# Kernel tuning notes

Hardware: AMD Instinct MI355X
Metric: run time of the kernel (lower is better)

## Reference

```python
import jax, jax.numpy as jnp
import numpy as np

L = 3          # layers
D = 256        # hidden_dim
H = 4          # heads
F = 1024       # ffn_size
IMG = (64, 32) # img_dim
S = IMG[0] * IMG[1]
DK = D // H    # key/query head dim
V = 2 * D      # double_v_dim value dim
DV = V // H    # value head dim
B = 2


def _rel_pos():
    # rotary angles, repeated pairwise as in get_rel_pos
    angle = 1.0 / (10000.0 ** jnp.linspace(0.0, 1.0, DK // 2))
    angle = jnp.repeat(angle, 2)                                  # [DK]
    idx = jnp.arange(S, dtype=jnp.float32)
    sin = jnp.sin(idx[:, None] * angle[None, :])                  # [S, DK]
    cos = jnp.cos(idx[:, None] * angle[None, :])
    # per-head causal decay mask, row-normalized by sqrt(rowsum)
    decay = jnp.log(1.0 - 2.0 ** (-5.0 - jnp.arange(H, dtype=jnp.float32)))  # [H]
    diff = idx[:, None] - idx[None, :]                            # [S, S]
    mask = jnp.where(diff >= 0, jnp.exp(diff[None, :, :] * decay[:, None, None]), 0.0)
    mask = mask / jnp.sqrt(mask.sum(-1, keepdims=True))           # [H, S, S]
    return sin, cos, mask


def _theta_shift(x, sin, cos):
    # x: [B, H, S, DK]; rotate-every-two rotary embedding
    x1, x2 = x[..., ::2], x[..., 1::2]
    rot = jnp.stack([-x2, x1], axis=-1).reshape(x.shape)
    return x * cos + rot * sin


def _ln(x, w, b, eps=1e-5):
    mu = x.mean(-1, keepdims=True)
    var = ((x - mu) ** 2).mean(-1, keepdims=True)
    return (x - mu) / jnp.sqrt(var + eps) * w + b


def _retention(x, sin, cos, mask, Wq, Wk, Wv, Wg, Wo):
    b, s, _ = x.shape
    q = (x @ Wq).reshape(b, s, H, DK).transpose(0, 2, 1, 3)
    k = (x @ Wk).reshape(b, s, H, DK).transpose(0, 2, 1, 3) * (DK ** -0.5)
    v = (x @ Wv).reshape(b, s, H, DV).transpose(0, 2, 1, 3)
    g = x @ Wg                                                    # [b, s, V]
    qr = _theta_shift(q, sin, cos)
    kr = _theta_shift(k, sin, cos)
    qk = jnp.einsum('bhsd,bhtd->bhst', qr, kr) * mask[None]
    denom = jnp.clip(jnp.abs(qk).sum(-1, keepdims=True), 1.0, None)
    qk = qk / jax.lax.stop_gradient(denom)
    o = jnp.einsum('bhst,bhtv->bhsv', qk, v)                      # [b, H, s, DV]
    o = o * jax.lax.rsqrt((o ** 2).mean(-1, keepdims=True) + 1e-6)  # per-head RMSNorm
    o = o.transpose(0, 2, 1, 3).reshape(b, s, V)
    o = (g * jax.nn.sigmoid(g)) * o                               # swish gate
    return o @ Wo


def setup_inputs():
    key = jax.random.key(0)
    ks = jax.random.split(key, 16)
    sc = 0.02
    return {
        'x': jax.random.normal(ks[0], (B, S, D), jnp.float32),
        'Wq': jax.random.normal(ks[1], (L, D, D), jnp.float32) * sc,
        'Wk': jax.random.normal(ks[2], (L, D, D), jnp.float32) * sc,
        'Wv': jax.random.normal(ks[3], (L, D, V), jnp.float32) * sc,
        'Wg': jax.random.normal(ks[4], (L, D, V), jnp.float32) * sc,
        'Wo': jax.random.normal(ks[5], (L, V, D), jnp.float32) * sc,
        'ln1_w': jnp.ones((L, D), jnp.float32),
        'ln1_b': jnp.zeros((L, D), jnp.float32),
        'ln2_w': jnp.ones((L, D), jnp.float32),
        'ln2_b': jnp.zeros((L, D), jnp.float32),
        'W1': jax.random.normal(ks[6], (L, D, F), jnp.float32) * sc,
        'b1': jnp.zeros((L, F), jnp.float32),
        'W2': jax.random.normal(ks[7], (L, F, D), jnp.float32) * sc,
        'b2': jnp.zeros((L, D), jnp.float32),
    }


def reference(x, Wq, Wk, Wv, Wg, Wo, ln1_w, ln1_b, ln2_w, ln2_b, W1, b1, W2, b2):
    sin, cos, mask = _rel_pos()
    for i in range(L):
        y = _retention(_ln(x, ln1_w[i], ln1_b[i]), sin, cos, mask,
                       Wq[i], Wk[i], Wv[i], Wg[i], Wo[i]) + x
        h = _ln(y, ln2_w[i], ln2_b[i])
        x = (jax.nn.gelu(h @ W1[i] + b1[i], approximate=False) @ W2[i] + b2[i]) + y
    return x.reshape(x.shape[0], IMG[0], IMG[1], D)
```

## Files before the change

### kernel.cpp

```cpp
#include <hip/hip_runtime.h>
#include <hip/hip_bf16.h>
#include <cstddef>
#include <cmath>
#include <algorithm>

#define SEQ 2048
#define DMODEL 256
#define NHEAD 4
#define DK 64
#define VDIM 512
#define DV 128
#define NB 2
#define FDIM 1024
#define NROWS (NB*SEQ)
#define QKVGN 1536
#define NSLOT 144

typedef unsigned short u16;
typedef __attribute__((ext_vector_type(8))) short short8;
typedef __attribute__((ext_vector_type(4))) short short4v;
typedef __attribute__((ext_vector_type(4))) float f32x4;

static __device__ __forceinline__ u16 f2b(float f) {
    union { float f; unsigned u; } c; c.f = f;
    unsigned r = c.u + 0x7fffu + ((c.u >> 16) & 1u);
    return (u16)(r >> 16);
}
static __device__ __forceinline__ float b2f(u16 u) {
    union { unsigned u; float f; } c; c.u = ((unsigned)u) << 16; return c.f;
}

static __device__ __forceinline__ f32x4 mfma16_bf16(short4v a, short4v b, f32x4 c) {
    return __builtin_amdgcn_mfma_f32_16x16x16bf16_1k(a, b, c, 0, 0, 0);
}

static __device__ __forceinline__ short4v pack_bf16x4(float a0, float a1, float a2, float a3) {
    union { short4v v; unsigned u[2]; } z;
    union { __hip_bfloat162 h; unsigned u; } p0, p1;
    p0.h = __float22bfloat162_rn(make_float2(a0, a1));
    p1.h = __float22bfloat162_rn(make_float2(a2, a3));
    z.u[0] = p0.u; z.u[1] = p1.u;
    return z.v;
}

#define GLOAD_LDS16(GP, LP) \
    __builtin_amdgcn_global_load_lds((const __attribute__((address_space(1))) void*)(GP), \
                                     (__attribute__((address_space(3))) void*)(LP), 16, 0, 0)

__global__ void tables_kernel(float* __restrict__ sint, float* __restrict__ cost)
{
    int idx = blockIdx.x * 256 + threadIdx.x;
    if (idx >= SEQ * DK) return;
    int s = idx >> 6, d = idx & 63;
    int j = d >> 1;
    float a = powf(10000.f, -(float)j / 31.f);
    float arg = (float)s * a;
    sint[idx] = sinf(arg);
    cost[idx] = cosf(arg);
}

__global__ __launch_bounds__(256) void wconv_kernel(const float* __restrict__ in,
                                                    u16* __restrict__ out, int K, int N,
                                                    size_t in_lstride, size_t out_lstride)
{
    __shared__ float tile[32][33];
    int n0 = blockIdx.x * 32, k0 = blockIdx.y * 32;
    const float* inz = in + (size_t)blockIdx.z * in_lstride;
    u16* outz = out + (size_t)blockIdx.z * out_lstride;
    int tx = threadIdx.x, ty = threadIdx.y;
    #pragma unroll
    for (int r = 0; r < 4; ++r) {
        int kr = ty + r * 8;
        tile[kr][tx] = inz[(size_t)(k0 + kr) * N + n0 + tx];
    }
    __syncthreads();
    #pragma unroll
    for (int r = 0; r < 4; ++r) {
        int nr = ty + r * 8;
        outz[(size_t)(n0 + nr) * K + k0 + tx] = f2b(tile[tx][nr]);
    }
}

__global__ __launch_bounds__(256) void ln_kernel(const float* __restrict__ x,
                                                 const float* __restrict__ w,
                                                 const float* __restrict__ b,
                                                 u16* __restrict__ o)
{
    int row = blockIdx.x * 4 + (threadIdx.x >> 6);
    int lane = threadIdx.x & 63;
    size_t base = (size_t)row * DMODEL + lane * 4;
    f32x4 v = *(const f32x4*)(x + base);
    float s  = v[0] + v[1] + v[2] + v[3];
    float s2 = v[0]*v[0] + v[1]*v[1] + v[2]*v[2] + v[3]*v[3];
    #pragma unroll
    for (int st = 1; st < 64; st <<= 1) { s += __shfl_xor(s, st); s2 += __shfl_xor(s2, st); }
    float mu = s * (1.f / 256.f);
    float var = s2 * (1.f / 256.f) - mu * mu;
    float rstd = rsqrtf(var + 1e-5f);
    f32x4 wv = *(const f32x4*)(w + lane * 4);
    f32x4 bv = *(const f32x4*)(b + lane * 4);
    f32x4 r = (v - mu) * rstd * wv + bv;
    *(short4v*)(o + base) = pack_bf16x4(r[0], r[1], r[2], r[3]);
}

template<int NPART, int HASBIAS>
__global__ __launch_bounds__(256) void lncomb_kernel(const u16* __restrict__ pW,
                                                     const float* __restrict__ bias,
                                                     const float* __restrict__ res,
                                                     const float* __restrict__ w,
                                                     const float* __restrict__ b,
                                                     float* __restrict__ yout,
                                                     u16* __restrict__ o)
{
    int row = blockIdx.x * 4 + (threadIdx.x >> 6);
    int lane = threadIdx.x & 63;
    size_t base = (size_t)row * DMODEL + lane * 4;
    const size_t PS = (size_t)NROWS * DMODEL;
    f32x4 v = *(const f32x4*)(res + base);
    #pragma unroll
    for (int k = 0; k < NPART; ++k) {
        short4v sv = *(const short4v*)(pW + base + k * PS);
        v[0] += b2f((u16)sv[0]); v[1] += b2f((u16)sv[1]);
        v[2] += b2f((u16)sv[2]); v[3] += b2f((u16)sv[3]);
    }
    if (HASBIAS) v += *(const f32x4*)(bias + lane * 4);
    *(f32x4*)(yout + base) = v;
    float s  = v[0] + v[1] + v[2] + v[3];
    float s2 = v[0]*v[0] + v[1]*v[1] + v[2]*v[2] + v[3]*v[3];
    #pragma unroll
    for (int st = 1; st < 64; st <<= 1) { s += __shfl_xor(s, st); s2 += __shfl_xor(s2, st); }
    float mu = s * (1.f / 256.f);
    float var = s2 * (1.f / 256.f) - mu * mu;
    float rstd = rsqrtf(var + 1e-5f);
    f32x4 wv = *(const f32x4*)(w + lane * 4);
    f32x4 bv = *(const f32x4*)(b + lane * 4);
    f32x4 r = (v - mu) * rstd * wv + bv;
    *(short4v*)(o + base) = pack_bf16x4(r[0], r[1], r[2], r[3]);
}

__global__ __launch_bounds__(256) void comb4_kernel(const u16* __restrict__ pW,
                                                    const float* __restrict__ bias,
                                                    const float* __restrict__ yb,
                                                    float* __restrict__ out)
{
    int row = blockIdx.x;
    int t = threadIdx.x;
    size_t i = (size_t)row * DMODEL + t;
    const size_t PS = (size_t)NROWS * DMODEL;
    out[i] = b2f(pW[i]) + b2f(pW[i + PS]) + b2f(pW[i + 2 * PS]) + b2f(pW[i + 3 * PS]) + bias[t] + yb[i];
}

template<int BIAS, int GELU, int ROT, int OUTBF, int SPLIT, int VT>
__global__ __launch_bounds__(256) void gemm64(const u16* __restrict__ A,
                                              const u16* __restrict__ Bt,
                                              void* __restrict__ Cout,
                                              const float* __restrict__ bias,
                                              const float* __restrict__ sint,
                                              const float* __restrict__ cost,
                                              u16* __restrict__ vtout,
                                              int M, int N, int K, int kslice)
{
    __shared__ __align__(16) u16 As[64 * 64];
    __shared__ __align__(16) u16 Bs[64 * 64];
    int bx = blockIdx.x, by = blockIdx.y;
    int tid = threadIdx.x;
    int wave = tid >> 6, lane = tid & 63;
    int wm = wave & 1, wn = wave >> 1;
    int l15 = lane & 15, lg = lane >> 4;
    int kb0 = SPLIT ? blockIdx.z * kslice : 0;
    int kcnt = SPLIT ? kslice : K;

    int L0 = wave * 64 + lane;
    int r0 = L0 >> 3, c0g = (L0 & 7) ^ ((r0 >> 1) & 7);
    int L1 = 256 + wave * 64 + lane;
    int r1 = L1 >> 3, c1g = (L1 & 7) ^ ((r1 >> 1) & 7);
    const u16* Ag0 = A + (size_t)(by * 64 + r0) * K + kb0 + c0g * 8;
    const u16* Ag1 = A + (size_t)(by * 64 + r1) * K + kb0 + c1g * 8;
    const u16* Bg0 = Bt + (size_t)(bx * 64 + r0) * K + kb0 + c0g * 8;
    const u16* Bg1 = Bt + (size_t)(bx * 64 + r1) * K + kb0 + c1g * 8;
    u16* Asw0 = &As[wave * 512];
    u16* Asw1 = &As[2048 + wave * 512];
    u16* Bsw0 = &Bs[wave * 512];
    u16* Bsw1 = &Bs[2048 + wave * 512];

    f32x4 acc[2][2] = {};
    for (int k0 = 0; k0 < kcnt; k0 += 64) {
        GLOAD_LDS16(Ag0 + k0, Asw0);
        GLOAD_LDS16(Ag1 + k0, Asw1);
        GLOAD_LDS16(Bg0 + k0, Bsw0);
        GLOAD_LDS16(Bg1 + k0, Bsw1);
        __syncthreads();
        #pragma unroll
        for (int kk = 0; kk < 2; ++kk) {
            short8 af[2], bf[2];
            #pragma unroll
            for (int i = 0; i < 2; ++i) {
                int ra = wm * 32 + i * 16 + l15;
                int rb = wn * 32 + i * 16 + l15;
                af[i] = *(const short8*)&As[ra * 64 + ((kk * 4 + lg) ^ ((ra >> 1) & 7)) * 8];
                bf[i] = *(const short8*)&Bs[rb * 64 + ((kk * 4 + lg) ^ ((rb >> 1) & 7)) * 8];
            }
            #pragma unroll
            for (int mi = 0; mi < 2; ++mi)
                #pragma unroll
                for (int ni = 0; ni < 2; ++ni)
                    acc[mi][ni] = __builtin_amdgcn_mfma_f32_16x16x32_bf16(af[mi], bf[ni], acc[mi][ni], 0, 0, 0);
        }
        __syncthreads();
    }

    float* Cf = (float*)Cout;
    u16* Ch = (u16*)Cout;
    u16* Chs = (u16*)Cout;
    #pragma unroll
    for (int mi = 0; mi < 2; ++mi)
        #pragma unroll
        for (int ni = 0; ni < 2; ++ni) {
            int colb = bx * 64 + wn * 32 + ni * 16;
            if (VT && colb >= 512 && colb < 1024) {
                int col = colb + l15;
                int z = ((by >> 5) << 2) + ((col - 512) >> 7);
                int dv = (col - 512) & 127;
                int s0b = (by * 64 + wm * 32) & (SEQ - 1);
                short4v pk = pack_bf16x4(acc[mi][ni][0], acc[mi][ni][1], acc[mi][ni][2], acc[mi][ni][3]);
                *(short4v*)(vtout + (size_t)(z * DV + dv) * SEQ + s0b + lg * 8 + mi * 4) = pk;
            } else {
                #pragma unroll
                for (int r = 0; r < 4; ++r) {
                    int row = by * 64 + wm * 32 + mi * 16 + lg * 4 + r;
                    int col = colb + l15;
                    float v = acc[mi][ni][r];
                    if (ROT) {
                        float pv = __shfl_xor(v, 1);
                        if (col < 512) {
                            int s = row & (SEQ - 1);
                            int dk = col & 63;
                            float c = cost[(s << 6) + dk], sn = sint[(s << 6) + dk];
                            float rv = (col & 1) ? (v * c + pv * sn) : (v * c - pv * sn);
                            v = (col < 256) ? rv : rv * 0.125f;
                        }
                    }
                    if (BIAS) v += bias[col];
                    if (GELU) v = 0.5f * v * (1.f + erff(v * 0.70710678118654752f));
                    if (SPLIT)      Chs[(size_t)blockIdx.z * M * N + (size_t)row * N + col] = f2b(v);
                    else if (OUTBF) Ch[(size_t)row * N + col] = f2b(v);
                    else            Cf[(size_t)row * N + col] = v;
                }
            }
        }
}

__global__ __launch_bounds__(256) void retention_p1(
    const u16* __restrict__ qkvg, const u16* __restrict__ vt,
    u16* __restrict__ po, float* __restrict__ pden)
{
    __shared__ __align__(16) u16 Klds[2][2048];
    __shared__ __align__(16) u16 Vlds[2][4096];

    int bid = blockIdx.x;
    int bh = bid & 7;
    int f = bid >> 3;
    int a = 0, base = 0;
    while (f >= base + 4 * (a + 1)) { base += 4 * (a + 1); ++a; }
    int segs = f - base;
    int qt64 = 4 * a + segs / (a + 1);
    int ch = segs % (a + 1);
    int b = bh >> 2, h = bh & 3;
    int slot = bh * NSLOT + f;

    int tid = threadIdx.x;
    int wave = tid >> 6, lane = tid & 63;
    int wq = wave;
    int l15 = lane & 15, lg = lane >> 4;

    float rgeo = 1.f - exp2f(-5.f - (float)h);
    float dec2 = log2f(rgeo);
    float step = exp2f(dec2 * -32.f);

    const u16* qbase  = qkvg + (size_t)b * SEQ * QKVGN + h * 64;
    const u16* kbase  = qbase + 256;
    const u16* vtg    = vt + (size_t)bh * DV * SEQ;

    int q0w = qt64 * 64 + wq * 16;
    short8 qf0 = *(const short8*)(qbase + (size_t)(q0w + l15) * QKVGN + lg * 8);
    short8 qf1 = *(const short8*)(qbase + (size_t)(q0w + l15) * QKVGN + 32 + lg * 8);

    int tb = ch * 8;
    int t_last = (ch == a) ? (2 * qt64 + 1) : (tb + 7);
    int hasdiag = (ch == a);

    float rinv  = exp2f(-dec2);
    float r16   = exp2f(dec2 * -16.f);
    float et00 = exp2f(dec2 * -(float)(tb * 32 + lg * 4));
    float et01 = et00 * rinv;
    float et02 = et01 * rinv;
    float et03 = et02 * rinv;
    float et10 = et00 * r16, et11 = et01 * r16, et12 = et02 * r16, et13 = et03 * r16;

    f32x4 oacc0 = {0.f,0.f,0.f,0.f}, oacc1 = {0.f,0.f,0.f,0.f};
    f32x4 oacc2 = {0.f,0.f,0.f,0.f}, oacc3 = {0.f,0.f,0.f,0.f};
    f32x4 oacc4 = {0.f,0.f,0.f,0.f}, oacc5 = {0.f,0.f,0.f,0.f};
    f32x4 oacc6 = {0.f,0.f,0.f,0.f}, oacc7 = {0.f,0.f,0.f,0.f};
    float den_l = 0.f;

#define STAGE(BUF, TI) do { \
    int t0_ = (TI) * 32; \
    _Pragma("unroll") \
    for (int ii = 0; ii < 3; ++ii) { \
        int inst_ = wave * 3 + ii; \
        if (inst_ < 4) { \
            const u16* g_ = kbase + (size_t)(t0_ + (lane & 31)) * QKVGN + (2 * inst_ + (lane >> 5)) * 8; \
            GLOAD_LDS16(g_, &Klds[BUF][inst_ * 512]); \
        } else { \
            int j_ = inst_ - 4; \
            const u16* g_ = vtg + (size_t)(j_ * 16 + (lane >> 2)) * SEQ + t0_ + (lane & 3) * 8; \
            GLOAD_LDS16(g_, &Vlds[BUF][j_ * 512]); \
        } \
    } \
} while (0)

#define BODY(BUF, T0, DIAG) do { \
    const u16* kb_ = &Klds[BUF][0]; \
    const u16* vb_ = &Vlds[BUF][0]; \
    short8 k00 = *(const short8*)(kb_ + (lg    ) * 256 + l15 * 8); \
    short8 k01 = *(const short8*)(kb_ + (4 + lg) * 256 + l15 * 8); \
    short8 k10 = *(const short8*)(kb_ + (lg    ) * 256 + (16 + l15) * 8); \
    short8 k11 = *(const short8*)(kb_ + (4 + lg) * 256 + (16 + l15) * 8); \
    short8 V0 = *(const short8*)(vb_ + (      l15) * 32 + lg * 8); \
    short8 V1 = *(const short8*)(vb_ + (16 +  l15) * 32 + lg * 8); \
    short8 V2 = *(const short8*)(vb_ + (32 +  l15) * 32 + lg * 8); \
    short8 V3 = *(const short8*)(vb_ + (48 +  l15) * 32 + lg * 8); \
    short8 V4 = *(const short8*)(vb_ + (64 +  l15) * 32 + lg * 8); \
    short8 V5 = *(const short8*)(vb_ + (80 +  l15) * 32 + lg * 8); \
    short8 V6 = *(const short8*)(vb_ + (96 +  l15) * 32 + lg * 8); \
    short8 V7 = *(const short8*)(vb_ + (112 + l15) * 32 + lg * 8); \
    f32x4 s0 = {0.f,0.f,0.f,0.f}, s1 = {0.f,0.f,0.f,0.f}; \
    s0 = __builtin_amdgcn_mfma_f32_16x16x32_bf16(k00, qf0, s0, 0, 0, 0); \
    s0 = __builtin_amdgcn_mfma_f32_16x16x32_bf16(k01, qf1, s0, 0, 0, 0); \
    s1 = __builtin_amdgcn_mfma_f32_16x16x32_bf16(k10, qf0, s1, 0, 0, 0); \
    s1 = __builtin_amdgcn_mfma_f32_16x16x32_bf16(k11, qf1, s1, 0, 0, 0); \
    float a0 = s0[0] * et00, a1 = s0[1] * et01, a2 = s0[2] * et02, a3 = s0[3] * et03; \
    float c0 = s1[0] * et10, c1 = s1[1] * et11, c2 = s1[2] * et12, c3 = s1[3] * et13; \
    if (DIAG) { \
        int qr_ = q0w + l15; \
        int tg_ = (T0) + lg * 4; \
        a0 = (tg_ +  0 <= qr_) ? a0 : 0.f;  a1 = (tg_ +  1 <= qr_) ? a1 : 0.f; \
        a2 = (tg_ +  2 <= qr_) ? a2 : 0.f;  a3 = (tg_ +  3 <= qr_) ? a3 : 0.f; \
        c0 = (tg_ + 16 <= qr_) ? c0 : 0.f;  c1 = (tg_ + 17 <= qr_) ? c1 : 0.f; \
        c2 = (tg_ + 18 <= qr_) ? c2 : 0.f;  c3 = (tg_ + 19 <= qr_) ? c3 : 0.f; \
    } \
    den_l += fabsf(a0) + fabsf(a1) + fabsf(a2) + fabsf(a3) \
           + fabsf(c0) + fabsf(c1) + fabsf(c2) + fabsf(c3); \
    short4v pa0 = pack_bf16x4(a0, a1, a2, a3); \
    short4v pa1 = pack_bf16x4(c0, c1, c2, c3); \
    short4v v0l = __builtin_shufflevector(V0, V0, 0, 1, 2, 3), v0h = __builtin_shufflevector(V0, V0, 4, 5, 6, 7); \
    short4v v1l = __builtin_shufflevector(V1, V1, 0, 1, 2, 3), v1h = __builtin_shufflevector(V1, V1, 4, 5, 6, 7); \
    short4v v2l = __builtin_shufflevector(V2, V2, 0, 1, 2, 3), v2h = __builtin_shufflevector(V2, V2, 4, 5, 6, 7); \
    short4v v3l = __builtin_shufflevector(V3, V3, 0, 1, 2, 3), v3h = __builtin_shufflevector(V3, V3, 4, 5, 6, 7); \
    short4v v4l = __builtin_shufflevector(V4, V4, 0, 1, 2, 3), v4h = __builtin_shufflevector(V4, V4, 4, 5, 6, 7); \
    short4v v5l = __builtin_shufflevector(V5, V5, 0, 1, 2, 3), v5h = __builtin_shufflevector(V5, V5, 4, 5, 6, 7); \
    short4v v6l = __builtin_shufflevector(V6, V6, 0, 1, 2, 3), v6h = __builtin_shufflevector(V6, V6, 4, 5, 6, 7); \
    short4v v7l = __builtin_shufflevector(V7, V7, 0, 1, 2, 3), v7h = __builtin_shufflevector(V7, V7, 4, 5, 6, 7); \
    oacc0 = mfma16_bf16(pa0, v0l, oacc0); oacc0 = mfma16_bf16(pa1, v0h, oacc0); \
    oacc1 = mfma16_bf16(pa0, v1l, oacc1); oacc1 = mfma16_bf16(pa1, v1h, oacc1); \
    oacc2 = mfma16_bf16(pa0, v2l, oacc2); oacc2 = mfma16_bf16(pa1, v2h, oacc2); \
    oacc3 = mfma16_bf16(pa0, v3l, oacc3); oacc3 = mfma16_bf16(pa1, v3h, oacc3); \
    oacc4 = mfma16_bf16(pa0, v4l, oacc4); oacc4 = mfma16_bf16(pa1, v4h, oacc4); \
    oacc5 = mfma16_bf16(pa0, v5l, oacc5); oacc5 = mfma16_bf16(pa1, v5h, oacc5); \
    oacc6 = mfma16_bf16(pa0, v6l, oacc6); oacc6 = mfma16_bf16(pa1, v6h, oacc6); \
    oacc7 = mfma16_bf16(pa0, v7l, oacc7); oacc7 = mfma16_bf16(pa1, v7h, oacc7); \
    et00 *= step; et01 *= step; et02 *= step; et03 *= step; \
    et10 *= step; et11 *= step; et12 *= step; et13 *= step; \
} while (0)

    int ti = tb;
    STAGE(0, tb);
    __syncthreads();
    for (; ti + 2 <= t_last; ti += 2) {
        STAGE(1, ti + 1);
        BODY(0, ti * 32, 0);
        __syncthreads();
        STAGE(0, ti + 2);
        BODY(1, (ti + 1) * 32, 0);
        __syncthreads();
    }
    if (ti < t_last) {
        STAGE(1, ti + 1);
        BODY(0, ti * 32, hasdiag);
        __syncthreads();
        BODY(1, (ti + 1) * 32, hasdiag);
    } else {
        BODY(0, ti * 32, hasdiag);
    }
#undef STAGE
#undef BODY

    den_l += __shfl_xor(den_l, 16);
    den_l += __shfl_xor(den_l, 32);
    if (lane < 16)
        pden[(size_t)slot * 64 + wq * 16 + l15] = den_l;

    u16* pobase = po + (size_t)slot * (64 * 128) + (wq * 16 + lg * 4) * 128 + l15;
    #pragma unroll
    for (int r = 0; r < 4; ++r) {
        pobase[r * 128 +   0] = f2b(oacc0[r]);
        pobase[r * 128 +  16] = f2b(oacc1[r]);
        pobase[r * 128 +  32] = f2b(oacc2[r]);
        pobase[r * 128 +  48] = f2b(oacc3[r]);
        pobase[r * 128 +  64] = f2b(oacc4[r]);
        pobase[r * 128 +  80] = f2b(oacc5[r]);
        pobase[r * 128 +  96] = f2b(oacc6[r]);
        pobase[r * 128 + 112] = f2b(oacc7[r]);
    }
}

__global__ __launch_bounds__(256) void retention_p2(
    const u16* __restrict__ po, const float* __restrict__ pden,
    const u16* __restrict__ qkvg, u16* __restrict__ og)
{
    int bid = blockIdx.x;
    int bh = bid & 7;
    int qt64 = bid >> 3;
    int b = bh >> 2, h = bh & 3;
    int aa = qt64 >> 2, rr = qt64 & 3;
    int sbase = bh * NSLOT + qt64 + 2 * aa * (aa - 1) + rr * aa;
    int nch = aa + 1;
    int t = threadIdx.x;
    int row = t >> 2, c0 = (t & 3) * 32;
    int q = qt64 * 64 + row;

    float den = 0.f;
    for (int k = 0; k < nch; ++k) den += pden[(size_t)(sbase + k) * 64 + row];
    float acc[32];
    #pragma unroll
    for (int j = 0; j < 32; ++j) acc[j] = 0.f;
    for (int k = 0; k < nch; ++k) {
        const u16* p = po + (size_t)(sbase + k) * (64 * 128) + row * 128 + c0;
        #pragma unroll
        for (int j = 0; j < 32; ++j) acc[j] += b2f(p[j]);
    }
    float rgeo = 1.f - exp2f(-5.f - (float)h);
    float dec2 = log2f(rgeo);
    float rp1 = exp2f(dec2 * (float)(q + 1));
    float cs = (1.f - rp1) / (1.f - rgeo);
    float invs = rsqrtf(cs);
    float eqv = exp2f(dec2 * (float)q);
    float d = fmaxf(den * eqv * invs, 1.f);
    float scl = eqv * invs / d;
    float ss = 0.f;
    #pragma unroll
    for (int j = 0; j < 32; ++j) { float v = acc[j] * scl; acc[j] = v; ss += v * v; }
    ss += __shfl_xor(ss, 1); ss += __shfl_xor(ss, 2);
    float rms = rsqrtf(ss * (1.f / DV) + 1e-6f);

    const u16* gbase = qkvg + ((size_t)(b * SEQ + q)) * QKVGN + 1024 + h * DV + c0;
    u16* obase = og + ((size_t)(b * SEQ + q)) * VDIM + h * DV + c0;
    #pragma unroll
    for (int j = 0; j < 32; ++j) {
        float gv = b2f(gbase[j]);
        float sig = 1.f / (1.f + __expf(-gv));
        obase[j] = f2b(gv * sig * acc[j] * rms);
    }
}

extern "C" void kernel_launch(void* const* d_in, const int* in_sizes, int n_in,
                              void* d_out, int out_size, void* d_ws, size_t ws_size,
                              hipStream_t stream)
{
    const float* x0    = (const float*)d_in[0];
    const float* Wq    = (const float*)d_in[1];
    const float* Wk    = (const float*)d_in[2];
    const float* Wv    = (const float*)d_in[3];
    const float* Wg    = (const float*)d_in[4];
    const float* Wo    = (const float*)d_in[5];
    const float* ln1w  = (const float*)d_in[6];
    const float* ln1b  = (const float*)d_in[7];
    const float* ln2w  = (const float*)d_in[8];
    const float* ln2b  = (const float*)d_in[9];
    const float* W1    = (const float*)d_in[10];
    const float* b1    = (const float*)d_in[11];
    const float* W2    = (const float*)d_in[12];
    const float* b2    = (const float*)d_in[13];

    char* ws = (char*)d_ws;
    size_t off = 0;
    auto alloc = [&](size_t bytes) { char* p = ws + off; off += (bytes + 255) & ~(size_t)255; return p; };

    float* sin_t = (float*)alloc(SEQ * DK * 4);
    float* cos_t = (float*)alloc(SEQ * DK * 4);
    u16* wqkvg_t = (u16*)alloc((size_t)3 * QKVGN * DMODEL * 2);
    u16* wo_t    = (u16*)alloc((size_t)3 * DMODEL * VDIM * 2);
    u16* w1_t    = (u16*)alloc((size_t)3 * FDIM * DMODEL * 2);
    u16* w2_t    = (u16*)alloc((size_t)3 * DMODEL * FDIM * 2);
    u16* qkvg    = (u16*)alloc((size_t)NROWS * QKVGN * 2);
    u16* xln     = (u16*)alloc((size_t)NROWS * DMODEL * 2);
    u16* vt      = (u16*)alloc((size_t)NB * NHEAD * DV * SEQ * 2);
    float* yb    = (float*)alloc((size_t)NROWS * DMODEL * 4);
    float* xbuf  = (float*)alloc((size_t)NROWS * DMODEL * 4);
    u16* po      = (u16*)alloc((size_t)8 * NSLOT * 64 * 128 * 2);
    float* pden  = (float*)alloc((size_t)8 * NSLOT * 64 * 4);
    u16* ff1 = qkvg;
    u16* h2  = xln;
    u16* ogb = vt;
    u16* pWh = po;

    tables_kernel<<<(SEQ * DK + 255) / 256, 256, 0, stream>>>(sin_t, cos_t);
    dim3 tb(32, 8);
    const size_t WLQ = (size_t)QKVGN * DMODEL;
    wconv_kernel<<<dim3(8, 8, 3),  tb, 0, stream>>>(Wq, wqkvg_t,              DMODEL, DMODEL, (size_t)DMODEL*DMODEL, WLQ);
    wconv_kernel<<<dim3(8, 8, 3),  tb, 0, stream>>>(Wk, wqkvg_t + 256 * 256,  DMODEL, DMODEL, (size_t)DMODEL*DMODEL, WLQ);
    wconv_kernel<<<dim3(16, 8, 3), tb, 0, stream>>>(Wv, wqkvg_t + 512 * 256,  DMODEL, VDIM,   (size_t)DMODEL*VDIM,   WLQ);
    wconv_kernel<<<dim3(16, 8, 3), tb, 0, stream>>>(Wg, wqkvg_t + 1024 * 256, DMODEL, VDIM,   (size_t)DMODEL*VDIM,   WLQ);
    wconv_kernel<<<dim3(8, 16, 3), tb, 0, stream>>>(Wo, wo_t, VDIM,   DMODEL, (size_t)VDIM*DMODEL,   (size_t)VDIM*DMODEL);
    wconv_kernel<<<dim3(32, 8, 3), tb, 0, stream>>>(W1, w1_t, DMODEL, FDIM,   (size_t)DMODEL*FDIM,   (size_t)DMODEL*FDIM);
    wconv_kernel<<<dim3(8, 32, 3), tb, 0, stream>>>(W2, w2_t, FDIM,   DMODEL, (size_t)FDIM*DMODEL,   (size_t)FDIM*DMODEL);

    ln_kernel<<<NROWS / 4, 256, 0, stream>>>(x0, ln1w, ln1b, xln);

    const float* xres = x0;
    for (int i = 0; i < 3; ++i) {
        const u16* wqkvgi = wqkvg_t + (size_t)i * QKVGN * DMODEL;
        const u16* woi = wo_t + (size_t)i * DMODEL * VDIM;
        const u16* w1i = w1_t + (size_t)i * FDIM * DMODEL;
        const u16* w2i = w2_t + (size_t)i * DMODEL * FDIM;

        gemm64<0,0,1,1,0,1><<<dim3(QKVGN/64, NROWS/64), 256, 0, stream>>>(
            xln, wqkvgi, qkvg, nullptr, sin_t, cos_t, vt, NROWS, QKVGN, DMODEL, 0);

        retention_p1<<<dim3(NSLOT * NB * NHEAD), 256, 0, stream>>>(qkvg, vt, po, pden);
        retention_p2<<<dim3((SEQ/64) * NB * NHEAD), 256, 0, stream>>>(po, pden, qkvg, ogb);

        gemm64<0,0,0,0,1,0><<<dim3(DMODEL/64, NROWS/64, 4), 256, 0, stream>>>(
            ogb, woi, pWh, nullptr, nullptr, nullptr, nullptr, NROWS, DMODEL, VDIM, 128);
        lncomb_kernel<4,0><<<NROWS / 4, 256, 0, stream>>>(pWh, nullptr, xres,
            ln2w + i * DMODEL, ln2b + i * DMODEL, yb, h2);

        gemm64<1,1,0,1,0,0><<<dim3(FDIM/64, NROWS/64), 256, 0, stream>>>(
            h2, w1i, ff1, b1 + (size_t)i * FDIM, nullptr, nullptr, nullptr, NROWS, FDIM, DMODEL, 0);

        gemm64<0,0,0,0,1,0><<<dim3(DMODEL/64, NROWS/64, 4), 256, 0, stream>>>(
            ff1, w2i, pWh, nullptr, nullptr, nullptr, nullptr, NROWS, DMODEL, FDIM, 256);

        if (i < 2) {
            lncomb_kernel<4,1><<<NROWS / 4, 256, 0, stream>>>(pWh, b2 + (size_t)i * DMODEL, yb,
                ln1w + (i + 1) * DMODEL, ln1b + (i + 1) * DMODEL, xbuf, xln);
            xres = xbuf;
        } else {
            comb4_kernel<<<NROWS, 256, 0, stream>>>(pWh, b2 + (size_t)i * DMODEL, yb, (float*)d_out);
        }
    }
}
```

Before: 263.5 us.

## Double-buffer GEMM tiles and use partial vmcnt waits to overlap loads

The 64x64 GEMM gets double-buffered LDS tiles, so the next K-tile's global-to-LDS loads are issued before computing on the current one. Full __syncthreads are replaced with explicit s_waitcnt vmcnt(N) plus raw s_barrier, and the retention kernel gets the same treatment, so only the oldest loads are waited on. This is meant to hide global load latency behind MFMA work. It doubles GEMM LDS use, which may reduce occupancy, and correctness depends on the hand-counted vmcnt values matching the number of loads issued per stage.

```diff
diff --git a/kernel.cpp b/kernel.cpp
--- a/kernel.cpp
+++ b/kernel.cpp
@@ -47,6 +47,13 @@
     __builtin_amdgcn_global_load_lds((const __attribute__((address_space(1))) void*)(GP), \
                                      (__attribute__((address_space(3))) void*)(LP), 16, 0, 0)
 
+#define WAITV4_BAR do { asm volatile("s_waitcnt vmcnt(4)" ::: "memory"); \
+    __builtin_amdgcn_sched_barrier(0); __builtin_amdgcn_s_barrier(); } while (0)
+#define WAITV3_BAR do { asm volatile("s_waitcnt vmcnt(3)" ::: "memory"); \
+    __builtin_amdgcn_sched_barrier(0); __builtin_amdgcn_s_barrier(); } while (0)
+#define WAITV0_BAR do { asm volatile("s_waitcnt vmcnt(0)" ::: "memory"); \
+    __builtin_amdgcn_sched_barrier(0); __builtin_amdgcn_s_barrier(); } while (0)
+
 __global__ void tables_kernel(float* __restrict__ sint, float* __restrict__ cost)
 {
     int idx = blockIdx.x * 256 + threadIdx.x;
@@ -160,8 +167,8 @@
                                               u16* __restrict__ vtout,
                                               int M, int N, int K, int kslice)
 {
-    __shared__ __align__(16) u16 As[64 * 64];
-    __shared__ __align__(16) u16 Bs[64 * 64];
+    __shared__ __align__(16) u16 As[2][64 * 64];
+    __shared__ __align__(16) u16 Bs[2][64 * 64];
     int bx = blockIdx.x, by = blockIdx.y;
     int tid = threadIdx.x;
     int wave = tid >> 6, lane = tid & 63;
@@ -178,18 +185,25 @@
     const u16* Ag1 = A + (size_t)(by * 64 + r1) * K + kb0 + c1g * 8;
     const u16* Bg0 = Bt + (size_t)(bx * 64 + r0) * K + kb0 + c0g * 8;
     const u16* Bg1 = Bt + (size_t)(bx * 64 + r1) * K + kb0 + c1g * 8;
-    u16* Asw0 = &As[wave * 512];
-    u16* Asw1 = &As[2048 + wave * 512];
-    u16* Bsw0 = &Bs[wave * 512];
-    u16* Bsw1 = &Bs[2048 + wave * 512];
+
+#define GSTAGE(BUF, KOFF) do { \
+    GLOAD_LDS16(Ag0 + (KOFF), &As[BUF][wave * 512]); \
+    GLOAD_LDS16(Ag1 + (KOFF), &As[BUF][2048 + wave * 512]); \
+    GLOAD_LDS16(Bg0 + (KOFF), &Bs[BUF][wave * 512]); \
+    GLOAD_LDS16(Bg1 + (KOFF), &Bs[BUF][2048 + wave * 512]); \
+} while (0)
 
     f32x4 acc[2][2] = {};
-    for (int k0 = 0; k0 < kcnt; k0 += 64) {
-        GLOAD_LDS16(Ag0 + k0, Asw0);
-        GLOAD_LDS16(Ag1 + k0, Asw1);
-        GLOAD_LDS16(Bg0 + k0, Bsw0);
-        GLOAD_LDS16(Bg1 + k0, Bsw1);
-        __syncthreads();
+    GSTAGE(0, 0);
+    int cur = 0;
+    for (int k0 = 0; k0 < kcnt; k0 += 64, cur ^= 1) {
+        bool more = (k0 + 64 < kcnt);
+        if (more) {
+            GSTAGE(cur ^ 1, k0 + 64);
+            WAITV4_BAR;
+        } else {
+            WAITV0_BAR;
+        }
         #pragma unroll
         for (int kk = 0; kk < 2; ++kk) {
             short8 af[2], bf[2];
@@ -197,8 +211,8 @@
             for (int i = 0; i < 2; ++i) {
                 int ra = wm * 32 + i * 16 + l15;
                 int rb = wn * 32 + i * 16 + l15;
-                af[i] = *(const short8*)&As[ra * 64 + ((kk * 4 + lg) ^ ((ra >> 1) & 7)) * 8];
-                bf[i] = *(const short8*)&Bs[rb * 64 + ((kk * 4 + lg) ^ ((rb >> 1) & 7)) * 8];
+                af[i] = *(const short8*)&As[cur][ra * 64 + ((kk * 4 + lg) ^ ((ra >> 1) & 7)) * 8];
+                bf[i] = *(const short8*)&Bs[cur][rb * 64 + ((kk * 4 + lg) ^ ((rb >> 1) & 7)) * 8];
             }
             #pragma unroll
             for (int mi = 0; mi < 2; ++mi)
@@ -206,8 +220,9 @@
                 for (int ni = 0; ni < 2; ++ni)
                     acc[mi][ni] = __builtin_amdgcn_mfma_f32_16x16x32_bf16(af[mi], bf[ni], acc[mi][ni], 0, 0, 0);
         }
-        __syncthreads();
-    }
+        if (more) __builtin_amdgcn_s_barrier();
+    }
+#undef GSTAGE
 
     float* Cf = (float*)Cout;
     u16* Ch = (u16*)Cout;
@@ -375,21 +390,24 @@
 
     int ti = tb;
     STAGE(0, tb);
-    __syncthreads();
     for (; ti + 2 <= t_last; ti += 2) {
         STAGE(1, ti + 1);
+        WAITV3_BAR;
         BODY(0, ti * 32, 0);
-        __syncthreads();
+        __builtin_amdgcn_s_barrier();
         STAGE(0, ti + 2);
+        WAITV3_BAR;
         BODY(1, (ti + 1) * 32, 0);
-        __syncthreads();
+        __builtin_amdgcn_s_barrier();
     }
     if (ti < t_last) {
         STAGE(1, ti + 1);
+        WAITV3_BAR;
         BODY(0, ti * 32, hasdiag);
-        __syncthreads();
+        WAITV0_BAR;
         BODY(1, (ti + 1) * 32, hasdiag);
     } else {
+        WAITV0_BAR;
         BODY(0, ti * 32, hasdiag);
     }
 #undef STAGE
```

Measured after the change: 271.1 us. +2.9%, slower.
